# Performance work log

Measured on AMD Instinct MI355X. Metric: run time of the kernel, lower is better.

## Reference

```python
import jax, jax.numpy as jnp
import numpy as np

D_MODEL = 1024
N_HEADS = 16
FF_DIM = 4096
EPS = 1e-05


def setup_inputs() -> dict:
    key = jax.random.key(0)
    ks = jax.random.split(key, 8)
    B, T, E, F = 4, 2048, D_MODEL, FF_DIM
    s = 0.02
    return {
        "encoder_input": jax.random.normal(ks[0], (B, T, E), jnp.float32),
        "source_padding_masks": jax.random.randint(ks[1], (B, T), 0, 2, jnp.int32),
        "Wq": jax.random.normal(ks[2], (E, E), jnp.float32) * s,
        "Wk": jax.random.normal(ks[3], (E, E), jnp.float32) * s,
        "Wv": jax.random.normal(ks[4], (E, E), jnp.float32) * s,
        "Wo": jax.random.normal(ks[5], (E, E), jnp.float32) * s,
        "w1": jax.random.normal(ks[6], (F, E), jnp.float32) * s,
        "b1": jnp.zeros((F,), jnp.float32),
        "w2": jax.random.normal(ks[7], (E, F), jnp.float32) * s,
        "b2": jnp.zeros((E,), jnp.float32),
        "ln_g": jnp.ones((E,), jnp.float32),
        "ln_b": jnp.zeros((E,), jnp.float32),
    }


def _layer_norm(x, g, b):
    # Faithful to the custom LayerNorm: unbiased std (ddof=1), eps added to sd.
    mean = jnp.mean(x, axis=-1, keepdims=True)
    sd = jnp.std(x, axis=-1, keepdims=True, ddof=1)
    return (x - mean) / (sd + EPS) * g + b


def reference(encoder_input, source_padding_masks, Wq, Wk, Wv, Wo, w1, b1, w2, b2, ln_g, ln_b):
    x = encoder_input
    B, T, E = x.shape
    H, hd = N_HEADS, E // N_HEADS

    q = (x @ Wq.T).reshape(B, T, H, hd).transpose(0, 2, 1, 3)  # [B,H,T,hd]
    k = (x @ Wk.T).reshape(B, T, H, hd).transpose(0, 2, 1, 3)
    v = (x @ Wv.T).reshape(B, T, H, hd).transpose(0, 2, 1, 3)

    scores = jnp.einsum("bhqd,bhkd->bhqk", q, k) / jnp.sqrt(jnp.float32(hd))
    key_mask = source_padding_masks[:, None, None, :]  # [B,1,1,T]
    scores = jnp.where(key_mask == 0, -jnp.inf, scores)
    attn = jax.nn.softmax(scores, axis=-1)
    attn = attn * source_padding_masks[:, None, :, None].astype(attn.dtype)  # query mask post-softmax

    ctx = jnp.einsum("bhqk,bhkd->bhqd", attn, v)
    ctx = ctx.transpose(0, 2, 1, 3).reshape(B, T, E)
    att_out = ctx @ Wo.T

    # residual block 1 (dropout is identity in eval)
    h = _layer_norm(att_out + x, ln_g, ln_b)

    ff = jax.nn.relu(h @ w1.T + b1) @ w2.T + b2
    # residual block 2 (same shared LayerNorm params)
    out = _layer_norm(ff + h, ln_g, ln_b)
    return out
```

## Files before the change

### kernel.cpp

```cpp
#include <hip/hip_runtime.h>
#include <hip/hip_bf16.h>


typedef __attribute__((ext_vector_type(8))) short  short8;
typedef __attribute__((ext_vector_type(4))) float  f32x4;
typedef __attribute__((ext_vector_type(4))) int    i32x4;
typedef __attribute__((ext_vector_type(4))) unsigned short u16x4;

__device__ inline float b2f(unsigned short u) {
    unsigned int x = ((unsigned int)u) << 16;
    return __builtin_bit_cast(float, x);
}
__device__ inline unsigned short f2b(float f) {
    return __builtin_bit_cast(unsigned short, __float2bfloat16(f));
}

__device__ inline void llds16(const unsigned short* g, unsigned short* l) {
    __builtin_amdgcn_global_load_lds(
        (const __attribute__((address_space(1))) unsigned int*)g,
        (__attribute__((address_space(3))) unsigned int*)l, 16, 0, 0);
}

__device__ inline int swz(int row, int col8) {
    return (row << 6) + (((col8 ^ (row >> 1)) & 7) << 3);
}

__global__ __launch_bounds__(256)
void cast_f32_bf16(const float* __restrict__ in, unsigned short* __restrict__ out,
                   int n4)
{
    int i = blockIdx.x * 256 + threadIdx.x;
    if (i >= n4) return;
    f32x4 v = *(const f32x4*)(in + (size_t)i * 4);
    u16x4 o;
    for (int j = 0; j < 4; ++j) o[j] = f2b(v[j]);
    *(u16x4*)(out + (size_t)i * 4) = o;
}

__global__ __launch_bounds__(256)
void mask_bf16(const int* __restrict__ m, unsigned short* __restrict__ mb, int n)
{
    int i = blockIdx.x * 256 + threadIdx.x;
    if (i < n) mb[i] = m[i] ? (unsigned short)0x3F80 : (unsigned short)0;
}

template <int BIAS, int RELU, int VT>
__global__ __launch_bounds__(256, 2)
void gemm_bt(const unsigned short* __restrict__ A,
             const unsigned short* __restrict__ W,
             const float* __restrict__ bias,
             const int* __restrict__ mask,
             unsigned short* __restrict__ C,
             int M, int N, int K)
{
    __shared__ __attribute__((aligned(16))) unsigned short a_s[128 * 64];
    __shared__ __attribute__((aligned(16))) unsigned short b_s[128 * 64];

    const int tid  = threadIdx.x;
    const int lane = tid & 63;
    const int w    = tid >> 6;
    const int ln   = lane & 15;
    const int quad = lane >> 4;
    const int wm   = w >> 1, wn = w & 1;
    const int bm   = blockIdx.y, bn = blockIdx.x;

    f32x4 acc[4][4] = {};

    const int nkt = K >> 6;
    for (int kt = 0; kt < nkt; ++kt) {
        for (int i = 0; i < 4; ++i) {
            int e   = i * 256 + tid;
            int row = e >> 3;
            int c8  = (e & 7) ^ ((e >> 4) & 7);
            llds16(A + (size_t)(bm * 128 + row) * K + kt * 64 + c8 * 8, &a_s[e * 8]);
            llds16(W + (size_t)(bn * 128 + row) * K + kt * 64 + c8 * 8, &b_s[e * 8]);
        }
        __syncthreads();
        for (int ks = 0; ks < 2; ++ks) {
            short8 af[4], bf_[4];
            for (int mt = 0; mt < 4; ++mt)
                af[mt] = *(const short8*)&a_s[swz(wm * 64 + mt * 16 + ln, ks * 4 + quad)];
            for (int nt = 0; nt < 4; ++nt)
                bf_[nt] = *(const short8*)&b_s[swz(wn * 64 + nt * 16 + ln, ks * 4 + quad)];
            for (int mt = 0; mt < 4; ++mt)
                for (int nt = 0; nt < 4; ++nt)
                    acc[mt][nt] = __builtin_amdgcn_mfma_f32_16x16x32_bf16(
                        af[mt], bf_[nt], acc[mt][nt], 0, 0, 0);
        }
        __syncthreads();
    }

    if (VT) {
        const int T2 = 2048, H2 = 16;
        for (int mt = 0; mt < 4; ++mt) {
            int row0 = bm * 128 + wm * 64 + mt * 16 + quad * 4;
            int bb = row0 >> 11, t0 = row0 & 2047;
            i32x4 mi = *(const i32x4*)&mask[bb * 2048 + t0];
            for (int nt = 0; nt < 4; ++nt) {
                int col = bn * 128 + wn * 64 + nt * 16 + ln;
                int hh2 = col >> 6, d = col & 63;
                u16x4 o;
                for (int r = 0; r < 4; ++r)
                    o[r] = mi[r] ? f2b(acc[mt][nt][r]) : (unsigned short)0;
                *(u16x4*)(C + ((size_t)((bb * H2 + hh2) * 64 + d)) * T2 + t0) = o;
            }
        }
    } else {
        for (int nt = 0; nt < 4; ++nt) {
            int col = bn * 128 + wn * 64 + nt * 16 + ln;
            float bv = 0.f;
            if (BIAS) bv = bias[col];
            for (int mt = 0; mt < 4; ++mt) {
                int row0 = bm * 128 + wm * 64 + mt * 16 + quad * 4;
                for (int r = 0; r < 4; ++r) {
                    float v = acc[mt][nt][r] + bv;
                    if (RELU) v = v > 0.f ? v : 0.f;
                    C[(size_t)(row0 + r) * N + col] = f2b(v);
                }
            }
        }
    }
}

__global__ __launch_bounds__(512, 2)
void flash_attn3(const unsigned short* __restrict__ Q,
                 const unsigned short* __restrict__ K,
                 const unsigned short* __restrict__ Vt,
                 const unsigned short* __restrict__ mb,
                 const int* __restrict__ mask,
                 unsigned short* __restrict__ O,
                 int T, int H, int E)
{
    __shared__ __attribute__((aligned(16))) unsigned short k_s[2][64 * 64];
    __shared__ __attribute__((aligned(16))) unsigned short v_s[2][64 * 64];
    __shared__ __attribute__((aligned(16))) unsigned short p_s[128 * 64];

    const int ord = blockIdx.x;
    const int wg  = (ord & 7) * 128 + (ord >> 3);
    const int qt  = wg & 15;
    const int h   = (wg >> 4) & 15;
    const int b   = wg >> 8;

    const int tid  = threadIdx.x;
    const int w    = tid >> 6;
    const int lane = tid & 63;
    const int ln   = lane & 15;
    const int quad = lane >> 4;
    const int q0   = qt * 128;
    const unsigned short* vt_b = Vt + (size_t)(b * H + h) * 64 * T;

    {
        int e = tid;
        int row = e >> 3;
        int c8  = (e & 7) ^ ((e >> 4) & 7);
        llds16(K + (size_t)(b * T + row) * E + h * 64 + c8 * 8, &k_s[0][e * 8]);
        llds16(vt_b + (size_t)row * T + c8 * 8, &v_s[0][e * 8]);
    }
    for (int i = 0; i < 2; ++i) {
        int e = i * 512 + tid;
        int row = e >> 3;
        int c8  = (e & 7) ^ ((e >> 4) & 7);
        llds16(Q + (size_t)(b * T + q0 + row) * E + h * 64 + c8 * 8, &p_s[e * 8]);
    }
    __syncthreads();
    short8 aq[2];
    aq[0] = *(const short8*)&p_s[w * 1024 + swz(ln, quad)];
    aq[1] = *(const short8*)&p_s[w * 1024 + swz(ln, 4 + quad)];

    f32x4 Oa[4] = {};
    f32x4 lacc = {};
    const float SCL = 0.125f * 1.44269504f;

    const int nkb = T >> 6;
    for (int kb = 0; kb < nkb; ++kb) {
        const int cur = kb & 1;
        if (kb + 1 < nkb) {
            int e = tid;
            int row = e >> 3;
            int c8  = (e & 7) ^ ((e >> 4) & 7);
            llds16(K + (size_t)(b * T + (kb + 1) * 64 + row) * E + h * 64 + c8 * 8,
                   &k_s[cur ^ 1][e * 8]);
            llds16(vt_b + (size_t)row * T + (kb + 1) * 64 + c8 * 8,
                   &v_s[cur ^ 1][e * 8]);
        }
        short8 mf0 = *(const short8*)&mb[b * T + kb * 64 + quad * 8];
        short8 mf1 = *(const short8*)&mb[b * T + kb * 64 + 32 + quad * 8];

        f32x4 S[4] = {};
        for (int ks = 0; ks < 2; ++ks)
            for (int nt = 0; nt < 4; ++nt) {
                short8 bf_ = *(const short8*)&k_s[cur][swz(nt * 16 + ln, ks * 4 + quad)];
                S[nt] = __builtin_amdgcn_mfma_f32_16x16x32_bf16(aq[ks], bf_, S[nt], 0, 0, 0);
            }
        for (int nt = 0; nt < 4; ++nt)
            for (int r = 0; r < 4; ++r) {
                float p = exp2f(S[nt][r] * SCL);
                p_s[w * 1024 + swz(quad * 4 + r, 2 * nt + (ln >> 3)) + (ln & 7)] = f2b(p);
            }
        short8 ap0 = *(const short8*)&p_s[w * 1024 + swz(ln, quad)];
        short8 ap1 = *(const short8*)&p_s[w * 1024 + swz(ln, 4 + quad)];
        lacc = __builtin_amdgcn_mfma_f32_16x16x32_bf16(ap0, mf0, lacc, 0, 0, 0);
        lacc = __builtin_amdgcn_mfma_f32_16x16x32_bf16(ap1, mf1, lacc, 0, 0, 0);
        for (int nt = 0; nt < 4; ++nt) {
            short8 bv0 = *(const short8*)&v_s[cur][swz(nt * 16 + ln, quad)];
            Oa[nt] = __builtin_amdgcn_mfma_f32_16x16x32_bf16(ap0, bv0, Oa[nt], 0, 0, 0);
            short8 bv1 = *(const short8*)&v_s[cur][swz(nt * 16 + ln, 4 + quad)];
            Oa[nt] = __builtin_amdgcn_mfma_f32_16x16x32_bf16(ap1, bv1, Oa[nt], 0, 0, 0);
        }
        __syncthreads();
    }

    for (int r = 0; r < 4; ++r) {
        int qrow = q0 + w * 16 + quad * 4 + r;
        float inv = mask[b * T + qrow] ? 1.f / lacc[r] : 0.f;
        for (int nt = 0; nt < 4; ++nt)
            O[(size_t)(b * T + qrow) * E + h * 64 + nt * 16 + ln] = f2b(Oa[nt][r] * inv);
    }
}

template <int R_F32, int O_F32>
__global__ __launch_bounds__(256, 4)
void ln_residual(const unsigned short* __restrict__ A,
                 const void* __restrict__ R,
                 const float* __restrict__ G,
                 const float* __restrict__ Bt,
                 void* __restrict__ Y, int E)
{
    const int row = blockIdx.x;
    const int tid = threadIdx.x;
    size_t base = (size_t)row * E + tid * 4;
    u16x4 a4 = *(const u16x4*)(A + base);
    float rv[4];
    if (R_F32) {
        f32x4 r4 = *(const f32x4*)((const float*)R + base);
        for (int j = 0; j < 4; ++j) rv[j] = r4[j];
    } else {
        u16x4 r4 = *(const u16x4*)((const unsigned short*)R + base);
        for (int j = 0; j < 4; ++j) rv[j] = b2f(r4[j]);
    }
    float v[4]; float s = 0.f, sq = 0.f;
    for (int j = 0; j < 4; ++j) {
        v[j] = b2f(a4[j]) + rv[j];
        s += v[j]; sq += v[j] * v[j];
    }
    for (int o = 32; o; o >>= 1) {
        s  += __shfl_xor(s, o, 64);
        sq += __shfl_xor(sq, o, 64);
    }
    __shared__ float red[8];
    int w = tid >> 6, lane = tid & 63;
    if (lane == 0) { red[w] = s; red[4 + w] = sq; }
    __syncthreads();
    s  = red[0] + red[1] + red[2] + red[3];
    sq = red[4] + red[5] + red[6] + red[7];
    float mean = s / E;
    float var  = (sq - s * mean) / (E - 1);
    var = fmaxf(var, 0.f);
    float inv = 1.f / (sqrtf(var) + 1e-5f);
    f32x4 g4 = *(const f32x4*)(G + tid * 4);
    f32x4 b4 = *(const f32x4*)(Bt + tid * 4);
    if (O_F32) {
        f32x4 o4;
        for (int j = 0; j < 4; ++j)
            o4[j] = (v[j] - mean) * inv * g4[j] + b4[j];
        *(f32x4*)((float*)Y + base) = o4;
    } else {
        u16x4 o4;
        for (int j = 0; j < 4; ++j)
            o4[j] = f2b((v[j] - mean) * inv * g4[j] + b4[j]);
        *(u16x4*)((unsigned short*)Y + base) = o4;
    }
}

extern "C" void kernel_launch(void* const* d_in, const int* in_sizes, int n_in,
                              void* d_out, int out_size, void* d_ws, size_t ws_size,
                              hipStream_t stream)
{
    const int B = 4, T = 2048, E = 1024, F = 4096, H = 16;
    const int M = B * T;

    const float* x  = (const float*)d_in[0];
    const int* mask = (const int*)d_in[1];
    const float* Wq = (const float*)d_in[2];
    const float* Wk = (const float*)d_in[3];
    const float* Wv = (const float*)d_in[4];
    const float* Wo = (const float*)d_in[5];
    const float* w1 = (const float*)d_in[6];
    const float* b1 = (const float*)d_in[7];
    const float* w2 = (const float*)d_in[8];
    const float* b2 = (const float*)d_in[9];
    const float* lg = (const float*)d_in[10];
    const float* lb = (const float*)d_in[11];
    float* out = (float*)d_out;

    char* ws = (char*)d_ws;
    const size_t MB = 1024 * 1024;
    unsigned short* xb  = (unsigned short*)(ws);
    unsigned short* q   = (unsigned short*)(ws + 16 * MB);
    unsigned short* kk  = (unsigned short*)(ws + 32 * MB);
    unsigned short* vt  = (unsigned short*)(ws + 48 * MB);
    unsigned short* ctx = (unsigned short*)(ws + 64 * MB);
    unsigned short* hh  = (unsigned short*)(ws + 80 * MB);
    unsigned short* mbf = hh;
    unsigned short* ff1 = (unsigned short*)(ws);
    unsigned short* ff2 = ctx;
    unsigned short* att = q;
    unsigned short* Wqb = (unsigned short*)(ws + 96 * MB);
    unsigned short* Wkb = (unsigned short*)(ws + 98 * MB);
    unsigned short* Wvb = (unsigned short*)(ws + 100 * MB);
    unsigned short* Wob = (unsigned short*)(ws + 102 * MB);
    unsigned short* w1b = (unsigned short*)(ws + 104 * MB);
    unsigned short* w2b = (unsigned short*)(ws + 112 * MB);

    dim3 blk(256);
    cast_f32_bf16<<<dim3(M * E / 4 / 256), blk, 0, stream>>>(x,  xb,  M * E / 4);
    cast_f32_bf16<<<dim3(E * E / 4 / 256), blk, 0, stream>>>(Wq, Wqb, E * E / 4);
    cast_f32_bf16<<<dim3(E * E / 4 / 256), blk, 0, stream>>>(Wk, Wkb, E * E / 4);
    cast_f32_bf16<<<dim3(E * E / 4 / 256), blk, 0, stream>>>(Wv, Wvb, E * E / 4);
    cast_f32_bf16<<<dim3(E * E / 4 / 256), blk, 0, stream>>>(Wo, Wob, E * E / 4);
    cast_f32_bf16<<<dim3(F * E / 4 / 256), blk, 0, stream>>>(w1, w1b, F * E / 4);
    cast_f32_bf16<<<dim3(F * E / 4 / 256), blk, 0, stream>>>(w2, w2b, F * E / 4);
    mask_bf16<<<dim3(M / 256), blk, 0, stream>>>(mask, mbf, M);

    gemm_bt<0, 0, 0><<<dim3(E / 128, M / 128), blk, 0, stream>>>(xb, Wqb, nullptr, nullptr, q,  M, E, E);
    gemm_bt<0, 0, 0><<<dim3(E / 128, M / 128), blk, 0, stream>>>(xb, Wkb, nullptr, nullptr, kk, M, E, E);
    gemm_bt<0, 0, 1><<<dim3(E / 128, M / 128), blk, 0, stream>>>(xb, Wvb, nullptr, mask, vt, M, E, E);
    flash_attn3<<<dim3((T / 128) * H * B), dim3(512), 0, stream>>>(q, kk, vt, mbf, mask, ctx, T, H, E);
    gemm_bt<0, 0, 0><<<dim3(E / 128, M / 128), blk, 0, stream>>>(ctx, Wob, nullptr, nullptr, att, M, E, E);
    ln_residual<1, 0><<<dim3(M), blk, 0, stream>>>(att, x, lg, lb, hh, E);
    gemm_bt<1, 1, 0><<<dim3(F / 128, M / 128), blk, 0, stream>>>(hh, w1b, b1, nullptr, ff1, M, F, E);
    gemm_bt<1, 0, 0><<<dim3(E / 128, M / 128), blk, 0, stream>>>(ff1, w2b, b2, nullptr, ff2, M, E, F);
    ln_residual<0, 1><<<dim3(M), blk, 0, stream>>>(ff2, hh, lg, lb, out, E);
}
```

Measured before the change: 576.4 us.

## Use 256x256 double-buffered GEMM tiles and fuse QKV projections into one launch

Replaces the 128x128 single-buffered GEMM with a 512-thread, 256x256-tile kernel. It double-buffers LDS, prefetching the next K tile while computing the current one, and raises wave priority around the MFMA block. The Q, K and V projections become one GEMM over the contiguous Wq/Wk/Wv bf16 buffers (N=3072), routing output segments to q, k and the masked transposed V. The larger tiles use about 128KB of LDS, likely one block per CU. The N=1024 GEMMs now launch only 128 blocks, which may leave CUs idle.

```diff
diff --git a/kernel.cpp b/kernel.cpp
--- a/kernel.cpp
+++ b/kernel.cpp
@@ -44,78 +44,121 @@
     if (i < n) mb[i] = m[i] ? (unsigned short)0x3F80 : (unsigned short)0;
 }
 
-template <int BIAS, int RELU, int VT>
-__global__ __launch_bounds__(256, 2)
-void gemm_bt(const unsigned short* __restrict__ A,
+template <int BIAS, int RELU, int QKV>
+__global__ __launch_bounds__(512, 2)
+void gemm256(const unsigned short* __restrict__ A,
              const unsigned short* __restrict__ W,
              const float* __restrict__ bias,
              const int* __restrict__ mask,
-             unsigned short* __restrict__ C,
+             unsigned short* __restrict__ C0,
+             unsigned short* __restrict__ C1,
+             unsigned short* __restrict__ C2,
              int M, int N, int K)
 {
-    __shared__ __attribute__((aligned(16))) unsigned short a_s[128 * 64];
-    __shared__ __attribute__((aligned(16))) unsigned short b_s[128 * 64];
+    __shared__ __attribute__((aligned(16))) unsigned short a_s[2][256 * 64];
+    __shared__ __attribute__((aligned(16))) unsigned short b_s[2][256 * 64];
 
     const int tid  = threadIdx.x;
     const int lane = tid & 63;
     const int w    = tid >> 6;
     const int ln   = lane & 15;
     const int quad = lane >> 4;
-    const int wm   = w >> 1, wn = w & 1;
+    const int wm   = w >> 2, wn = w & 3;
     const int bm   = blockIdx.y, bn = blockIdx.x;
 
-    f32x4 acc[4][4] = {};
-
-    const int nkt = K >> 6;
-    for (int kt = 0; kt < nkt; ++kt) {
+    f32x4 acc[8][4] = {};
+
+    auto stage = [&](int buf, int kt) {
+#pragma unroll
         for (int i = 0; i < 4; ++i) {
-            int e   = i * 256 + tid;
+            int e   = i * 512 + tid;
             int row = e >> 3;
             int c8  = (e & 7) ^ ((e >> 4) & 7);
-            llds16(A + (size_t)(bm * 128 + row) * K + kt * 64 + c8 * 8, &a_s[e * 8]);
-            llds16(W + (size_t)(bn * 128 + row) * K + kt * 64 + c8 * 8, &b_s[e * 8]);
-        }
-        __syncthreads();
+            llds16(A + (size_t)(bm * 256 + row) * K + kt * 64 + c8 * 8,
+                   &a_s[buf][e * 8]);
+            llds16(W + (size_t)(bn * 256 + row) * K + kt * 64 + c8 * 8,
+                   &b_s[buf][e * 8]);
+        }
+    };
+
+    const int nkt = K >> 6;
+    stage(0, 0);
+    for (int kt = 0; kt < nkt; ++kt) {
+        const int cur = kt & 1;
+        asm volatile("s_waitcnt vmcnt(0)" ::: "memory");
+        __builtin_amdgcn_s_barrier();
+        if (kt + 1 < nkt) stage(cur ^ 1, kt + 1);
+#pragma unroll
         for (int ks = 0; ks < 2; ++ks) {
-            short8 af[4], bf_[4];
-            for (int mt = 0; mt < 4; ++mt)
-                af[mt] = *(const short8*)&a_s[swz(wm * 64 + mt * 16 + ln, ks * 4 + quad)];
+            short8 af[8], bf_[4];
+#pragma unroll
+            for (int mt = 0; mt < 8; ++mt)
+                af[mt] = *(const short8*)&a_s[cur][swz(wm * 128 + mt * 16 + ln, ks * 4 + quad)];
+#pragma unroll
             for (int nt = 0; nt < 4; ++nt)
-                bf_[nt] = *(const short8*)&b_s[swz(wn * 64 + nt * 16 + ln, ks * 4 + quad)];
-            for (int mt = 0; mt < 4; ++mt)
+                bf_[nt] = *(const short8*)&b_s[cur][swz(wn * 64 + nt * 16 + ln, ks * 4 + quad)];
+            __builtin_amdgcn_s_setprio(1);
+#pragma unroll
+            for (int mt = 0; mt < 8; ++mt)
+#pragma unroll
                 for (int nt = 0; nt < 4; ++nt)
                     acc[mt][nt] = __builtin_amdgcn_mfma_f32_16x16x32_bf16(
                         af[mt], bf_[nt], acc[mt][nt], 0, 0, 0);
-        }
-        __syncthreads();
-    }
-
-    if (VT) {
-        const int T2 = 2048, H2 = 16;
-        for (int mt = 0; mt < 4; ++mt) {
-            int row0 = bm * 128 + wm * 64 + mt * 16 + quad * 4;
-            int bb = row0 >> 11, t0 = row0 & 2047;
-            i32x4 mi = *(const i32x4*)&mask[bb * 2048 + t0];
+            __builtin_amdgcn_s_setprio(0);
+        }
+    }
+
+    const int crow0 = bm * 256 + wm * 128;
+    const int ccol0 = bn * 256 + wn * 64;
+    if (QKV) {
+        const int seg  = bn >> 2;
+        const int lc0  = ccol0 & 1023;
+        if (seg < 2) {
+            unsigned short* C = seg == 0 ? C0 : C1;
+#pragma unroll
             for (int nt = 0; nt < 4; ++nt) {
-                int col = bn * 128 + wn * 64 + nt * 16 + ln;
-                int hh2 = col >> 6, d = col & 63;
-                u16x4 o;
-                for (int r = 0; r < 4; ++r)
-                    o[r] = mi[r] ? f2b(acc[mt][nt][r]) : (unsigned short)0;
-                *(u16x4*)(C + ((size_t)((bb * H2 + hh2) * 64 + d)) * T2 + t0) = o;
+                int col = lc0 + nt * 16 + ln;
+#pragma unroll
+                for (int mt = 0; mt < 8; ++mt) {
+                    int row0 = crow0 + mt * 16 + quad * 4;
+#pragma unroll
+                    for (int r = 0; r < 4; ++r)
+                        C[(size_t)(row0 + r) * 1024 + col] = f2b(acc[mt][nt][r]);
+                }
+            }
+        } else {
+            const int T2 = 2048, H2 = 16;
+#pragma unroll
+            for (int mt = 0; mt < 8; ++mt) {
+                int row0 = crow0 + mt * 16 + quad * 4;
+                int bb = row0 >> 11, t0 = row0 & 2047;
+                i32x4 mi = *(const i32x4*)&mask[bb * 2048 + t0];
+#pragma unroll
+                for (int nt = 0; nt < 4; ++nt) {
+                    int col = lc0 + nt * 16 + ln;
+                    int hh2 = col >> 6, d = col & 63;
+                    u16x4 o;
+#pragma unroll
+                    for (int r = 0; r < 4; ++r)
+                        o[r] = mi[r] ? f2b(acc[mt][nt][r]) : (unsigned short)0;
+                    *(u16x4*)(C2 + ((size_t)((bb * H2 + hh2) * 64 + d)) * T2 + t0) = o;
+                }
             }
         }
     } else {
+#pragma unroll
         for (int nt = 0; nt < 4; ++nt) {
-            int col = bn * 128 + wn * 64 + nt * 16 + ln;
+            int col = ccol0 + nt * 16 + ln;
             float bv = 0.f;
             if (BIAS) bv = bias[col];
-            for (int mt = 0; mt < 4; ++mt) {
-                int row0 = bm * 128 + wm * 64 + mt * 16 + quad * 4;
+#pragma unroll
+            for (int mt = 0; mt < 8; ++mt) {
+                int row0 = crow0 + mt * 16 + quad * 4;
+#pragma unroll
                 for (int r = 0; r < 4; ++r) {
                     float v = acc[mt][nt][r] + bv;
                     if (RELU) v = v > 0.f ? v : 0.f;
-                    C[(size_t)(row0 + r) * N + col] = f2b(v);
+                    C0[(size_t)(row0 + r) * N + col] = f2b(v);
                 }
             }
         }
@@ -322,13 +365,16 @@
     cast_f32_bf16<<<dim3(F * E / 4 / 256), blk, 0, stream>>>(w2, w2b, F * E / 4);
     mask_bf16<<<dim3(M / 256), blk, 0, stream>>>(mask, mbf, M);
 
-    gemm_bt<0, 0, 0><<<dim3(E / 128, M / 128), blk, 0, stream>>>(xb, Wqb, nullptr, nullptr, q,  M, E, E);
-    gemm_bt<0, 0, 0><<<dim3(E / 128, M / 128), blk, 0, stream>>>(xb, Wkb, nullptr, nullptr, kk, M, E, E);
-    gemm_bt<0, 0, 1><<<dim3(E / 128, M / 128), blk, 0, stream>>>(xb, Wvb, nullptr, mask, vt, M, E, E);
-    flash_attn3<<<dim3((T / 128) * H * B), dim3(512), 0, stream>>>(q, kk, vt, mbf, mask, ctx, T, H, E);
-    gemm_bt<0, 0, 0><<<dim3(E / 128, M / 128), blk, 0, stream>>>(ctx, Wob, nullptr, nullptr, att, M, E, E);
+    dim3 g512(512);
+    gemm256<0, 0, 1><<<dim3(3072 / 256, M / 256), g512, 0, stream>>>(
+        xb, Wqb, nullptr, mask, q, kk, vt, M, 3072, E);
+    flash_attn3<<<dim3((T / 128) * H * B), g512, 0, stream>>>(q, kk, vt, mbf, mask, ctx, T, H, E);
+    gemm256<0, 0, 0><<<dim3(E / 256, M / 256), g512, 0, stream>>>(
+        ctx, Wob, nullptr, nullptr, att, nullptr, nullptr, M, E, E);
     ln_residual<1, 0><<<dim3(M), blk, 0, stream>>>(att, x, lg, lb, hh, E);
-    gemm_bt<1, 1, 0><<<dim3(F / 128, M / 128), blk, 0, stream>>>(hh, w1b, b1, nullptr, ff1, M, F, E);
-    gemm_bt<1, 0, 0><<<dim3(E / 128, M / 128), blk, 0, stream>>>(ff1, w2b, b2, nullptr, ff2, M, E, F);
+    gemm256<1, 1, 0><<<dim3(F / 256, M / 256), g512, 0, stream>>>(
+        hh, w1b, b1, nullptr, ff1, nullptr, nullptr, M, F, E);
+    gemm256<1, 0, 0><<<dim3(E / 256, M / 256), g512, 0, stream>>>(
+        ff1, w2b, b2, nullptr, ff2, nullptr, nullptr, M, E, F);
     ln_residual<0, 1><<<dim3(M), blk, 0, stream>>>(ff2, hh, lg, lb, out, E);
 }
```

New measurement: 614.3 us. 1.07x slower.
